# Kernel tuning notes

Measured on AMD Instinct MI355X. Metric: run time of the kernel, lower is better.

## Reference

```python
import jax, jax.numpy as jnp
import numpy as np

VOCAB, D = 6000, 256  # vocab_size, units
B, L = 64, 2048


def setup_inputs() -> dict:
    key = jax.random.key(0)
    k1, k2, k3, k4, k5 = jax.random.split(key, 5)
    context = jax.random.randint(k1, (B, L), 0, VOCAB)  # 0 = pad/mask id
    emb = jax.random.normal(k2, (VOCAB, D), dtype=jnp.float32) * 0.05
    # Keras LSTM packs gates as [i, f, c, o] along the last axis (4*D)
    W = jax.random.normal(k3, (D, 4 * D), dtype=jnp.float32) * (1.0 / np.sqrt(D))
    U = jax.random.normal(k4, (D, 4 * D), dtype=jnp.float32) * (1.0 / np.sqrt(D))
    b = jnp.concatenate([
        jnp.zeros((D,), jnp.float32),
        jnp.ones((D,), jnp.float32),   # unit_forget_bias=True default in Keras
        jnp.zeros((2 * D,), jnp.float32),
    ])
    return {"context": context, "emb": emb, "W": W, "U": U, "b": b}


def reference(context, emb, W, U, b):
    mask = context != 0                       # (B, L) mask_zero semantics
    x = emb[context]                          # (B, L, D) embedding lookup
    xg = jnp.einsum("bld,dg->blg", x, W) + b  # (B, L, 4D) input-to-gate, precomputed

    h0 = jnp.zeros((context.shape[0], D), xg.dtype)
    c0 = h0

    def step(carry, inp):
        h, c = carry
        xg_t, m = inp                          # (B, 4D), (B,)
        g = xg_t + h @ U                       # (B, 4D)
        i, f, cand, o = jnp.split(g, 4, axis=-1)
        i = jax.nn.sigmoid(i)
        f = jax.nn.sigmoid(f)
        o = jax.nn.sigmoid(o)
        c_new = f * c + i * jnp.tanh(cand)
        h_new = o * jnp.tanh(c_new)
        m = m[:, None]
        # Keras masking: masked steps carry previous state/output forward
        h = jnp.where(m, h_new, h)
        c = jnp.where(m, c_new, c)
        return (h, c), h

    xs = (jnp.swapaxes(xg, 0, 1), jnp.swapaxes(mask, 0, 1))  # time-major for scan
    (_, _), hs = jax.lax.scan(step, (h0, c0), xs)
    return jnp.swapaxes(hs, 0, 1)             # (B, L, D)
```

## Files before the change

kernel.cpp:

```cpp
#include <hip/hip_runtime.h>
#include <hip/hip_bf16.h>


#define B_     64
#define L_     2048
#define D_     256
#define G4_    1024
#define VOCAB_ 6000

typedef short    s16x8 __attribute__((ext_vector_type(8)));
typedef float    f32x4 __attribute__((ext_vector_type(4)));
typedef unsigned u32x2 __attribute__((ext_vector_type(2)));
typedef unsigned u32x4 __attribute__((ext_vector_type(4)));

#define OFF_EMBB   0u
#define OFF_WT     3072000u
#define OFF_UF     3596288u
#define OFF_HTAG   4120576u
#define OFF_DONE   4251648u
#define OFF_XG     4251712u
#define WS_NEED    272687168u

#define HL_OFF     0
#define SG_OFF     8192
#define ROLE_OFF   25600
#define SMEM_TOTAL 90112

__global__ void prep_kernel(const float* __restrict__ emb,
                            const float* __restrict__ W,
                            const float* __restrict__ U,
                            __hip_bfloat16* __restrict__ embb,
                            __hip_bfloat16* __restrict__ Wt,
                            __hip_bfloat16* __restrict__ Ufrag) {
  const int stride = gridDim.x * blockDim.x;
  const int i0 = blockIdx.x * blockDim.x + threadIdx.x;
  for (int i = i0; i < VOCAB_ * D_; i += stride)
    embb[i] = __float2bfloat16(emb[i]);
  for (int i = i0; i < D_ * G4_; i += stride) {
    int k = i >> 10;
    int n = i & (G4_ - 1);
    Wt[n * D_ + k] = __float2bfloat16(W[i]);
  }
  for (int i = i0; i < 262144; i += stride) {
    int j  = i & 7;
    int l  = (i >> 3) & 63;
    int fr = i >> 9;
    int kk = fr & 7;
    int st = (fr >> 3) & 1;
    int w  = (fr >> 4) & 7;
    int qq = fr >> 7;
    int n = (w >> 1) * 256 + qq * 64 + (w & 1) * 32 + st * 16 + (l & 15);
    int k = kk * 32 + (l >> 4) * 8 + j;
    Ufrag[i] = __float2bfloat16(U[k * G4_ + n]);
  }
}

__global__ void mask_kernel(const int* __restrict__ ctx,
                            unsigned char* __restrict__ m8) {
  const int stride = gridDim.x * blockDim.x;
  for (int i = blockIdx.x * blockDim.x + threadIdx.x; i < B_ * L_; i += stride) {
    int b = i & 63, t = i >> 6;
    m8[t * 64 + b] = (ctx[b * L_ + t] != 0) ? 1 : 0;
  }
}

__device__ inline unsigned pk2(float a, float b) {
  return (unsigned)__bfloat16_as_ushort(__float2bfloat16(a)) |
         ((unsigned)__bfloat16_as_ushort(__float2bfloat16(b)) << 16);
}
__device__ inline float bl(unsigned u) {
  union { unsigned u; float f; } c; c.u = u << 16; return c.f;
}
__device__ inline float bh(unsigned u) {
  union { unsigned u; float f; } c; c.u = u & 0xffff0000u; return c.f;
}
__device__ inline float fsigmoid(float x) { return 1.f / (1.f + __expf(-x)); }
__device__ inline float ftanh(float x)    { return 1.f - 2.f / (__expf(2.f * x) + 1.f); }

__global__ __launch_bounds__(256, 2)
void xg_kernel(const int* __restrict__ ctx,
               const __hip_bfloat16* __restrict__ embb,
               const __hip_bfloat16* __restrict__ Wt,
               unsigned* __restrict__ xgw) {
  const int bid = blockIdx.x;
  const int Q   = bid & 3;
  const int g   = (bid >> 2) & 3;
  const int tc  = bid >> 4;
  const int tid = threadIdx.x;
  const int wv  = tid >> 6;
  const int l   = tid & 63;
  const int l15 = l & 15, lhi = l >> 4;
  const int row0 = g * 16;

  s16x8 bfr[8][4];
#pragma unroll
  for (int nt = 0; nt < 4; ++nt) {
    const int n = Q * 256 + wv * 64 + nt * 16 + l15;
    const __hip_bfloat16* wp = Wt + n * D_ + lhi * 8;
#pragma unroll
    for (int kk = 0; kk < 8; ++kk)
      bfr[kk][nt] = *(const s16x8*)(wp + kk * 32);
  }

  for (int tt = 0; tt < 64; ++tt) {
    const int t = tc * 64 + tt;
    const int tok = ctx[(row0 + l15) * L_ + t];
    const __hip_bfloat16* xp = embb + tok * D_ + lhi * 8;
    s16x8 af[8];
#pragma unroll
    for (int kk = 0; kk < 8; ++kk)
      af[kk] = *(const s16x8*)(xp + kk * 32);

    f32x4 acc[4];
#pragma unroll
    for (int nt = 0; nt < 4; ++nt) acc[nt] = (f32x4){0.f, 0.f, 0.f, 0.f};
#pragma unroll
    for (int kk = 0; kk < 8; ++kk)
#pragma unroll
      for (int nt = 0; nt < 4; ++nt)
        acc[nt] = __builtin_amdgcn_mfma_f32_16x16x32_bf16(af[kk], bfr[kk][nt], acc[nt], 0, 0, 0);

#pragma unroll
    for (int nt = 0; nt < 4; ++nt)
#pragma unroll
      for (int r = 0; r < 4; ++r) {
        float nb = __shfl_xor(acc[nt][r], 1);
        if (!(l15 & 1)) {
          unsigned v = pk2(acc[nt][r], nb);
          int em = lhi * 4 + r;
          int p  = nt * 8 + (l15 >> 1);
          size_t idx = ((((size_t)(t * 4 + g) * 4 + wv) * 16 + em) * 32 + p) * 4 + Q;
          xgw[idx] = v;
        }
      }
  }
}

__global__ __launch_bounds__(512, 1)
void scan_kernel(const float* __restrict__ bias,
                 const __hip_bfloat16* __restrict__ Ufrag,
                 const unsigned* __restrict__ xgw,
                 const unsigned char* __restrict__ mask8,
                 unsigned* __restrict__ donef,
                 char* __restrict__ htag,
                 float* __restrict__ out) {
  extern __shared__ __align__(16) char smem[];
  const int bid = blockIdx.x;
  const int tid = threadIdx.x;

  if (bid >= 16) {
    volatile int* hd = (volatile int*)(smem + ROLE_OFF);
    if (tid == 0) *hd = 0;
    __syncthreads();
    float v0 = (float)(tid + 1), v1 = v0 * 1.1f, v2 = v0 * 1.2f, v3 = v0 * 1.3f;
    for (int it = 0; it < (1 << 15); ++it) {
#pragma unroll
      for (int kk = 0; kk < 128; ++kk) {
        v0 = __builtin_fmaf(v0, 1.0000001f, 1.0e-7f);
        v1 = __builtin_fmaf(v1, 1.0000001f, 1.0e-7f);
        v2 = __builtin_fmaf(v2, 1.0000001f, 1.0e-7f);
        v3 = __builtin_fmaf(v3, 1.0000001f, 1.0e-7f);
      }
      if (tid == 0 && (it & 15) == 0) {
        u32x4 fa, fb, fc, fd;
        asm volatile(
            "global_load_dwordx4 %0, %4, off sc0 sc1\n\t"
            "global_load_dwordx4 %1, %4, off offset:16 sc0 sc1\n\t"
            "global_load_dwordx4 %2, %4, off offset:32 sc0 sc1\n\t"
            "global_load_dwordx4 %3, %4, off offset:48 sc0 sc1\n\t"
            "s_waitcnt vmcnt(0)"
            : "=&v"(fa), "=&v"(fb), "=&v"(fc), "=&v"(fd)
            : "v"(donef) : "memory");
        unsigned mn = fa.x;
        mn = fa.y < mn ? fa.y : mn; mn = fa.z < mn ? fa.z : mn; mn = fa.w < mn ? fa.w : mn;
        mn = fb.x < mn ? fb.x : mn; mn = fb.y < mn ? fb.y : mn;
        mn = fb.z < mn ? fb.z : mn; mn = fb.w < mn ? fb.w : mn;
        mn = fc.x < mn ? fc.x : mn; mn = fc.y < mn ? fc.y : mn;
        mn = fc.z < mn ? fc.z : mn; mn = fc.w < mn ? fc.w : mn;
        mn = fd.x < mn ? fd.x : mn; mn = fd.y < mn ? fd.y : mn;
        mn = fd.z < mn ? fd.z : mn; mn = fd.w < mn ? fd.w : mn;
        if (mn != 0u) *hd = 1;
      }
      if (*hd) break;
    }
    asm volatile("" :: "v"(v0), "v"(v1), "v"(v2), "v"(v3));
    return;
  }

  const int g = bid >> 2;
  const int q = bid & 3;
  const int row0 = g * 16;

  const int w   = tid >> 6;
  const int l   = tid & 63;
  const int l15 = l & 15, lhi = l >> 4;
  const int Q   = w >> 1, sgs = w & 1;
  const int em  = tid >> 5;
  const int e5  = tid & 31;

  float* sg = (float*)(smem + SG_OFF);
  char*  hl = smem + HL_OFF;
  const s16x8* uf = (const s16x8*)Ufrag;

  s16x8 ur[16];
#pragma unroll
  for (int kk = 0; kk < 8; ++kk)
#pragma unroll
    for (int st = 0; st < 2; ++st)
      ur[kk * 2 + st] = uf[((((q * 8 + w) * 2 + st) * 8) + kk) * 64 + l];

  float bq[4][2];
#pragma unroll
  for (int Qq = 0; Qq < 4; ++Qq) {
    bq[Qq][0] = bias[Qq * 256 + q * 64 + 2 * e5];
    bq[Qq][1] = bias[Qq * 256 + q * 64 + 2 * e5 + 1];
  }

  float cc[2] = {0.f, 0.f}, hh[2] = {0.f, 0.f};

  const int prow = w * 2 + (l >> 5);
  const int pswz = (prow & 7) << 4;
  const int swzf = (l15 & 7) << 4;

  for (int t = 0; t < L_; ++t) {
    const u32x4 xq = *(const u32x4*)(xgw +
        (((((size_t)t * 4 + g) * 4 + q) * 16 + em) * 32 + e5) * 4);
    const unsigned char mk = mask8[t * 64 + row0 + em];

    {
      const char* hp = htag + ((t + 1) & 1) * 65536 + (row0 + prow) * 1024 + (l & 31) * 32;
      const unsigned want = (unsigned)t;
      u32x4 qa, qb;
      int spins = 0;
      while (true) {
        asm volatile("global_load_dwordx4 %0, %2, off sc0 sc1\n\t"
                     "global_load_dwordx4 %1, %2, off offset:16 sc0 sc1\n\t"
                     "s_waitcnt vmcnt(0)"
                     : "=&v"(qa), "=&v"(qb) : "v"(hp) : "memory");
        unsigned mn = qa.y < qa.w ? qa.y : qa.w;
        mn = qb.y < mn ? qb.y : mn;
        mn = qb.w < mn ? qb.w : mn;
        if (__all((int)(mn >= want))) break;
        if (++spins > 16384) break;
      }
      union { unsigned u[4]; s16x8 v; } hcv;
      hcv.u[0] = qa.x; hcv.u[1] = qa.z; hcv.u[2] = qb.x; hcv.u[3] = qb.z;
      *(s16x8*)(hl + prow * 512 + (((l & 31) * 16) ^ pswz)) = hcv.v;
    }
    asm volatile("s_waitcnt lgkmcnt(0)" ::: "memory");
    __builtin_amdgcn_s_barrier();

    f32x4 acc0 = {0.f, 0.f, 0.f, 0.f}, acc1 = {0.f, 0.f, 0.f, 0.f};
    s16x8 hf[8];
#pragma unroll
    for (int kk = 0; kk < 8; ++kk)
      hf[kk] = *(const s16x8*)(hl + l15 * 512 + ((kk * 64 + lhi * 16) ^ swzf));
#pragma unroll
    for (int kk = 0; kk < 8; ++kk) {
      acc0 = __builtin_amdgcn_mfma_f32_16x16x32_bf16(hf[kk], ur[kk * 2 + 0], acc0, 0, 0, 0);
      acc1 = __builtin_amdgcn_mfma_f32_16x16x32_bf16(hf[kk], ur[kk * 2 + 1], acc1, 0, 0, 0);
    }

#pragma unroll
    for (int r = 0; r < 4; ++r) {
      sg[(Q * 16 + lhi * 4 + r) * 66 + sgs * 32 + l15]      = acc0[r];
      sg[(Q * 16 + lhi * 4 + r) * 66 + sgs * 32 + 16 + l15] = acc1[r];
    }
    asm volatile("s_waitcnt lgkmcnt(0)" ::: "memory");
    __builtin_amdgcn_s_barrier();

    {
      float gv[4][2];
#pragma unroll
      for (int Qq = 0; Qq < 4; ++Qq) {
        gv[Qq][0] = sg[(Qq * 16 + em) * 66 + 2 * e5];
        gv[Qq][1] = sg[(Qq * 16 + em) * 66 + 2 * e5 + 1];
      }
      const bool upd = (mk != 0);
      unsigned short hsv[2];
#pragma unroll
      for (int b = 0; b < 2; ++b) {
        float xi = b ? bh(xq.x) : bl(xq.x);
        float xf = b ? bh(xq.y) : bl(xq.y);
        float xc = b ? bh(xq.z) : bl(xq.z);
        float xo = b ? bh(xq.w) : bl(xq.w);
        float gi = gv[0][b] + xi + bq[0][b];
        float gf = gv[1][b] + xf + bq[1][b];
        float gc = gv[2][b] + xc + bq[2][b];
        float go = gv[3][b] + xo + bq[3][b];
        float i_ = fsigmoid(gi), f_ = fsigmoid(gf), o_ = fsigmoid(go);
        float cn = f_ * cc[b] + i_ * ftanh(gc);
        float hn = o_ * ftanh(cn);
        cc[b] = upd ? cn : cc[b];
        hh[b] = upd ? hn : hh[b];
        hsv[b] = __bfloat16_as_ushort(__float2bfloat16(hh[b]));
      }
      u32x2 gr;
      gr.x = (unsigned)hsv[0] | ((unsigned)hsv[1] << 16);
      gr.y = (unsigned)(t + 1);
      char* pw = htag + (t & 1) * 65536 + (row0 + em) * 1024 + (q * 32 + e5) * 8;
      asm volatile("global_store_dwordx2 %0, %1, off sc0 sc1"
                   :: "v"(pw), "v"(gr) : "memory");
      float* op = out + ((size_t)(row0 + em) * L_ + t) * D_ + q * 64 + 2 * e5;
      op[0] = hh[0];
      op[1] = hh[1];
    }
  }

  if (tid == 0) {
    unsigned one = 1u;
    unsigned* df = donef + bid;
    asm volatile("global_store_dword %0, %1, off sc0 sc1"
                 :: "v"(df), "v"(one) : "memory");
  }
}

extern "C" void kernel_launch(void* const* d_in, const int* in_sizes, int n_in,
                              void* d_out, int out_size, void* d_ws, size_t ws_size,
                              hipStream_t stream) {
  const int*   ctx  = (const int*)d_in[0];
  const float* emb  = (const float*)d_in[1];
  const float* W    = (const float*)d_in[2];
  const float* U    = (const float*)d_in[3];
  const float* bias = (const float*)d_in[4];
  float* out = (float*)d_out;

  char* ws = (char*)d_ws;
  __hip_bfloat16* embb = (__hip_bfloat16*)(ws + OFF_EMBB);
  __hip_bfloat16* Wt   = (__hip_bfloat16*)(ws + OFF_WT);
  __hip_bfloat16* Uf   = (__hip_bfloat16*)(ws + OFF_UF);
  char*           htag = ws + OFF_HTAG;
  unsigned*       donef = (unsigned*)(ws + OFF_DONE);
  unsigned*       xgw  = (unsigned*)(ws + OFF_XG);
  unsigned char*  m8   = (unsigned char*)(ws + OFF_WT);

  hipMemsetAsync(htag, 0, 131072, stream);
  hipMemsetAsync(donef, 0, 64, stream);

  hipFuncSetAttribute((const void*)scan_kernel,
                      hipFuncAttributeMaxDynamicSharedMemorySize, SMEM_TOTAL);

  prep_kernel<<<1024, 256, 0, stream>>>(emb, W, U, embb, Wt, Uf);
  xg_kernel<<<512, 256, 0, stream>>>(ctx, embb, Wt, xgw);
  mask_kernel<<<128, 256, 0, stream>>>(ctx, m8);
  scan_kernel<<<256, 512, SMEM_TOTAL, stream>>>(bias, Uf, xgw, m8, donef, htag, out);
}
```

Measured before the change: 4.685 ms.

## Cut scan to four blocks, each looping over all batch groups per step

The recurrent scan now runs on 4 worker blocks, one per hidden-column quarter, instead of 16. Each block walks the four 16-row batch groups in turn inside every timestep, keeping per-group cell and hidden state in registers. The intent is fewer blocks taking part in the cross-block flag handshake, with a smaller done-flag poll in the idle blocks. In exchange, each block does four times the serial matmul, barrier and gate work per step, which lengthens the per-step critical path.

```diff
diff --git a/kernel.cpp b/kernel.cpp
--- a/kernel.cpp
+++ b/kernel.cpp
@@ -148,7 +148,7 @@
   const int bid = blockIdx.x;
   const int tid = threadIdx.x;
 
-  if (bid >= 16) {
+  if (bid >= 4) {
     volatile int* hd = (volatile int*)(smem + ROLE_OFF);
     if (tid == 0) *hd = 0;
     __syncthreads();
@@ -162,23 +162,14 @@
         v3 = __builtin_fmaf(v3, 1.0000001f, 1.0e-7f);
       }
       if (tid == 0 && (it & 15) == 0) {
-        u32x4 fa, fb, fc, fd;
-        asm volatile(
-            "global_load_dwordx4 %0, %4, off sc0 sc1\n\t"
-            "global_load_dwordx4 %1, %4, off offset:16 sc0 sc1\n\t"
-            "global_load_dwordx4 %2, %4, off offset:32 sc0 sc1\n\t"
-            "global_load_dwordx4 %3, %4, off offset:48 sc0 sc1\n\t"
-            "s_waitcnt vmcnt(0)"
-            : "=&v"(fa), "=&v"(fb), "=&v"(fc), "=&v"(fd)
-            : "v"(donef) : "memory");
+        u32x4 fa;
+        asm volatile("global_load_dwordx4 %0, %1, off sc0 sc1\n\t"
+                     "s_waitcnt vmcnt(0)"
+                     : "=&v"(fa) : "v"(donef) : "memory");
         unsigned mn = fa.x;
-        mn = fa.y < mn ? fa.y : mn; mn = fa.z < mn ? fa.z : mn; mn = fa.w < mn ? fa.w : mn;
-        mn = fb.x < mn ? fb.x : mn; mn = fb.y < mn ? fb.y : mn;
-        mn = fb.z < mn ? fb.z : mn; mn = fb.w < mn ? fb.w : mn;
-        mn = fc.x < mn ? fc.x : mn; mn = fc.y < mn ? fc.y : mn;
-        mn = fc.z < mn ? fc.z : mn; mn = fc.w < mn ? fc.w : mn;
-        mn = fd.x < mn ? fd.x : mn; mn = fd.y < mn ? fd.y : mn;
-        mn = fd.z < mn ? fd.z : mn; mn = fd.w < mn ? fd.w : mn;
+        mn = fa.y < mn ? fa.y : mn;
+        mn = fa.z < mn ? fa.z : mn;
+        mn = fa.w < mn ? fa.w : mn;
         if (mn != 0u) *hd = 1;
       }
       if (*hd) break;
@@ -187,9 +178,7 @@
     return;
   }
 
-  const int g = bid >> 2;
-  const int q = bid & 3;
-  const int row0 = g * 16;
+  const int q = bid;
 
   const int w   = tid >> 6;
   const int l   = tid & 63;
@@ -216,100 +205,109 @@
     bq[Qq][1] = bias[Qq * 256 + q * 64 + 2 * e5 + 1];
   }
 
-  float cc[2] = {0.f, 0.f}, hh[2] = {0.f, 0.f};
+  float cc[4][2] = {{0.f, 0.f}, {0.f, 0.f}, {0.f, 0.f}, {0.f, 0.f}};
+  float hh[4][2] = {{0.f, 0.f}, {0.f, 0.f}, {0.f, 0.f}, {0.f, 0.f}};
 
   const int prow = w * 2 + (l >> 5);
   const int pswz = (prow & 7) << 4;
   const int swzf = (l15 & 7) << 4;
 
   for (int t = 0; t < L_; ++t) {
-    const u32x4 xq = *(const u32x4*)(xgw +
-        (((((size_t)t * 4 + g) * 4 + q) * 16 + em) * 32 + e5) * 4);
-    const unsigned char mk = mask8[t * 64 + row0 + em];
-
-    {
-      const char* hp = htag + ((t + 1) & 1) * 65536 + (row0 + prow) * 1024 + (l & 31) * 32;
-      const unsigned want = (unsigned)t;
-      u32x4 qa, qb;
-      int spins = 0;
-      while (true) {
-        asm volatile("global_load_dwordx4 %0, %2, off sc0 sc1\n\t"
-                     "global_load_dwordx4 %1, %2, off offset:16 sc0 sc1\n\t"
-                     "s_waitcnt vmcnt(0)"
-                     : "=&v"(qa), "=&v"(qb) : "v"(hp) : "memory");
-        unsigned mn = qa.y < qa.w ? qa.y : qa.w;
-        mn = qb.y < mn ? qb.y : mn;
-        mn = qb.w < mn ? qb.w : mn;
-        if (__all((int)(mn >= want))) break;
-        if (++spins > 16384) break;
-      }
-      union { unsigned u[4]; s16x8 v; } hcv;
-      hcv.u[0] = qa.x; hcv.u[1] = qa.z; hcv.u[2] = qb.x; hcv.u[3] = qb.z;
-      *(s16x8*)(hl + prow * 512 + (((l & 31) * 16) ^ pswz)) = hcv.v;
-    }
-    asm volatile("s_waitcnt lgkmcnt(0)" ::: "memory");
-    __builtin_amdgcn_s_barrier();
-
-    f32x4 acc0 = {0.f, 0.f, 0.f, 0.f}, acc1 = {0.f, 0.f, 0.f, 0.f};
-    s16x8 hf[8];
-#pragma unroll
-    for (int kk = 0; kk < 8; ++kk)
-      hf[kk] = *(const s16x8*)(hl + l15 * 512 + ((kk * 64 + lhi * 16) ^ swzf));
-#pragma unroll
-    for (int kk = 0; kk < 8; ++kk) {
-      acc0 = __builtin_amdgcn_mfma_f32_16x16x32_bf16(hf[kk], ur[kk * 2 + 0], acc0, 0, 0, 0);
-      acc1 = __builtin_amdgcn_mfma_f32_16x16x32_bf16(hf[kk], ur[kk * 2 + 1], acc1, 0, 0, 0);
-    }
-
-#pragma unroll
-    for (int r = 0; r < 4; ++r) {
-      sg[(Q * 16 + lhi * 4 + r) * 66 + sgs * 32 + l15]      = acc0[r];
-      sg[(Q * 16 + lhi * 4 + r) * 66 + sgs * 32 + 16 + l15] = acc1[r];
-    }
-    asm volatile("s_waitcnt lgkmcnt(0)" ::: "memory");
-    __builtin_amdgcn_s_barrier();
-
-    {
-      float gv[4][2];
-#pragma unroll
-      for (int Qq = 0; Qq < 4; ++Qq) {
-        gv[Qq][0] = sg[(Qq * 16 + em) * 66 + 2 * e5];
-        gv[Qq][1] = sg[(Qq * 16 + em) * 66 + 2 * e5 + 1];
-      }
-      const bool upd = (mk != 0);
-      unsigned short hsv[2];
-#pragma unroll
-      for (int b = 0; b < 2; ++b) {
-        float xi = b ? bh(xq.x) : bl(xq.x);
-        float xf = b ? bh(xq.y) : bl(xq.y);
-        float xc = b ? bh(xq.z) : bl(xq.z);
-        float xo = b ? bh(xq.w) : bl(xq.w);
-        float gi = gv[0][b] + xi + bq[0][b];
-        float gf = gv[1][b] + xf + bq[1][b];
-        float gc = gv[2][b] + xc + bq[2][b];
-        float go = gv[3][b] + xo + bq[3][b];
-        float i_ = fsigmoid(gi), f_ = fsigmoid(gf), o_ = fsigmoid(go);
-        float cn = f_ * cc[b] + i_ * ftanh(gc);
-        float hn = o_ * ftanh(cn);
-        cc[b] = upd ? cn : cc[b];
-        hh[b] = upd ? hn : hh[b];
-        hsv[b] = __bfloat16_as_ushort(__float2bfloat16(hh[b]));
-      }
-      u32x2 gr;
-      gr.x = (unsigned)hsv[0] | ((unsigned)hsv[1] << 16);
-      gr.y = (unsigned)(t + 1);
-      char* pw = htag + (t & 1) * 65536 + (row0 + em) * 1024 + (q * 32 + e5) * 8;
-      asm volatile("global_store_dwordx2 %0, %1, off sc0 sc1"
-                   :: "v"(pw), "v"(gr) : "memory");
-      float* op = out + ((size_t)(row0 + em) * L_ + t) * D_ + q * 64 + 2 * e5;
-      op[0] = hh[0];
-      op[1] = hh[1];
+    const unsigned want = (unsigned)t;
+    const int parR = (t + 1) & 1;
+    const int parW = t & 1;
+
+#pragma unroll
+    for (int G = 0; G < 4; ++G) {
+      const int row0 = G * 16;
+
+      const u32x4 xq = *(const u32x4*)(xgw +
+          (((((size_t)t * 4 + G) * 4 + q) * 16 + em) * 32 + e5) * 4);
+      const unsigned char mk = mask8[t * 64 + row0 + em];
+
+      {
+        const char* hp = htag + parR * 65536 + (row0 + prow) * 1024 + (l & 31) * 32;
+        u32x4 qa, qb;
+        int spins = 0;
+        while (true) {
+          asm volatile("global_load_dwordx4 %0, %2, off sc0 sc1\n\t"
+                       "global_load_dwordx4 %1, %2, off offset:16 sc0 sc1\n\t"
+                       "s_waitcnt vmcnt(0)"
+                       : "=&v"(qa), "=&v"(qb) : "v"(hp) : "memory");
+          unsigned mn = qa.y < qa.w ? qa.y : qa.w;
+          mn = qb.y < mn ? qb.y : mn;
+          mn = qb.w < mn ? qb.w : mn;
+          if (__all((int)(mn >= want))) break;
+          if (++spins > 16384) break;
+        }
+        union { unsigned u[4]; s16x8 v; } hcv;
+        hcv.u[0] = qa.x; hcv.u[1] = qa.z; hcv.u[2] = qb.x; hcv.u[3] = qb.z;
+        *(s16x8*)(hl + prow * 512 + (((l & 31) * 16) ^ pswz)) = hcv.v;
+      }
+      asm volatile("s_waitcnt lgkmcnt(0)" ::: "memory");
+      __builtin_amdgcn_s_barrier();
+
+      f32x4 acc0 = {0.f, 0.f, 0.f, 0.f}, acc1 = {0.f, 0.f, 0.f, 0.f};
+      s16x8 hf[8];
+#pragma unroll
+      for (int kk = 0; kk < 8; ++kk)
+        hf[kk] = *(const s16x8*)(hl + l15 * 512 + ((kk * 64 + lhi * 16) ^ swzf));
+#pragma unroll
+      for (int kk = 0; kk < 8; ++kk) {
+        acc0 = __builtin_amdgcn_mfma_f32_16x16x32_bf16(hf[kk], ur[kk * 2 + 0], acc0, 0, 0, 0);
+        acc1 = __builtin_amdgcn_mfma_f32_16x16x32_bf16(hf[kk], ur[kk * 2 + 1], acc1, 0, 0, 0);
+      }
+
+#pragma unroll
+      for (int r = 0; r < 4; ++r) {
+        sg[(Q * 16 + lhi * 4 + r) * 66 + sgs * 32 + l15]      = acc0[r];
+        sg[(Q * 16 + lhi * 4 + r) * 66 + sgs * 32 + 16 + l15] = acc1[r];
+      }
+      asm volatile("s_waitcnt lgkmcnt(0)" ::: "memory");
+      __builtin_amdgcn_s_barrier();
+
+      {
+        float gv[4][2];
+#pragma unroll
+        for (int Qq = 0; Qq < 4; ++Qq) {
+          gv[Qq][0] = sg[(Qq * 16 + em) * 66 + 2 * e5];
+          gv[Qq][1] = sg[(Qq * 16 + em) * 66 + 2 * e5 + 1];
+        }
+        const bool upd = (mk != 0);
+        unsigned short hsv[2];
+#pragma unroll
+        for (int b = 0; b < 2; ++b) {
+          float xi = b ? bh(xq.x) : bl(xq.x);
+          float xf = b ? bh(xq.y) : bl(xq.y);
+          float xc = b ? bh(xq.z) : bl(xq.z);
+          float xo = b ? bh(xq.w) : bl(xq.w);
+          float gi = gv[0][b] + xi + bq[0][b];
+          float gf = gv[1][b] + xf + bq[1][b];
+          float gc = gv[2][b] + xc + bq[2][b];
+          float go = gv[3][b] + xo + bq[3][b];
+          float i_ = fsigmoid(gi), f_ = fsigmoid(gf), o_ = fsigmoid(go);
+          float cn = f_ * cc[G][b] + i_ * ftanh(gc);
+          float hn = o_ * ftanh(cn);
+          cc[G][b] = upd ? cn : cc[G][b];
+          hh[G][b] = upd ? hn : hh[G][b];
+          hsv[b] = __bfloat16_as_ushort(__float2bfloat16(hh[G][b]));
+        }
+        u32x2 gr;
+        gr.x = (unsigned)hsv[0] | ((unsigned)hsv[1] << 16);
+        gr.y = (unsigned)(t + 1);
+        char* pw = htag + parW * 65536 + (row0 + em) * 1024 + (q * 32 + e5) * 8;
+        asm volatile("global_store_dwordx2 %0, %1, off sc0 sc1"
+                     :: "v"(pw), "v"(gr) : "memory");
+        float* op = out + ((size_t)(row0 + em) * L_ + t) * D_ + q * 64 + 2 * e5;
+        op[0] = hh[G][0];
+        op[1] = hh[G][1];
+      }
     }
   }
 
   if (tid == 0) {
     unsigned one = 1u;
-    unsigned* df = donef + bid;
+    unsigned* df = donef + q;
     asm volatile("global_store_dword %0, %1, off sc0 sc1"
                  :: "v"(df), "v"(one) : "memory");
   }
```

Result: slower. 15.76 ms (+236.4%).
